# Performance work log

Measured on AMD Instinct MI355X. Metric: run time of the kernel, lower is better.

The kernel has to match this reference:

```python
import jax, jax.numpy as jnp
import numpy as np

NUM_ITEMS = 100000
HIDDEN = 128
NNZ = 1600000


def setup_inputs() -> dict:
    key = jax.random.key(0)
    k1, k2, k3, k4, k5, k6 = jax.random.split(key, 6)
    item_embedding_table = jax.random.normal(k1, (NUM_ITEMS, HIDDEN), dtype=jnp.float32)
    adj_rows = jnp.sort(jax.random.randint(k2, (NNZ,), 0, NUM_ITEMS, dtype=jnp.int32))
    adj_cols = jax.random.randint(k3, (NNZ,), 0, NUM_ITEMS, dtype=jnp.int32)
    adj_vals = jax.random.uniform(k4, (NNZ,), dtype=jnp.float32)
    # nn.Linear default init (uniform in +-1/sqrt(fan_in)) approximated by scaled normal
    W_weight = jax.random.normal(k5, (HIDDEN, HIDDEN), dtype=jnp.float32) / np.sqrt(HIDDEN)
    W_bias = jax.random.normal(k6, (HIDDEN,), dtype=jnp.float32) * 0.01
    return {
        "item_embedding_table": item_embedding_table,
        "adj_rows": adj_rows,
        "adj_cols": adj_cols,
        "adj_vals": adj_vals,
        "W_weight": W_weight,
        "W_bias": W_bias,
    }


def reference(item_embedding_table, adj_rows, adj_cols, adj_vals, W_weight, W_bias):
    # support = W(x): x @ W^T + b   (nn.Linear convention: weight [out, in])
    support = jnp.einsum("nd,hd->nh", item_embedding_table, W_weight) + W_bias  # [N, H]
    # output = sparse_coo(adj) @ support, via gather + segment-sum scatter
    msgs = adj_vals[:, None] * support[adj_cols]  # [nnz, H]
    output = jax.ops.segment_sum(msgs, adj_rows, num_segments=NUM_ITEMS)  # [N, H]
    return output
```

## Files before the change

kernel.cpp:

```cpp
#include <hip/hip_runtime.h>
#include <hip/hip_fp16.h>

#define N_ITEMS 100000
#define HID 128
#define NNZ_T 1600000
#define PREPW_BLOCKS 64
#define RP_BLOCKS 391

typedef unsigned short ushort_t;
typedef unsigned int uint_t;
typedef short bf16x8 __attribute__((ext_vector_type(8)));
typedef float f32x4 __attribute__((ext_vector_type(4)));

static __device__ __forceinline__ ushort_t f32_to_bf16(float f) {
    uint_t u = __float_as_uint(f);
    uint_t r = (u + 0x7FFFu + ((u >> 16) & 1u)) >> 16;
    return (ushort_t)r;
}

__global__ void prep(const float* __restrict__ W, const int* __restrict__ rows,
                     ushort_t* __restrict__ Wb, int* __restrict__ row_ptr) {
    if (blockIdx.x < PREPW_BLOCKS) {
        int i = blockIdx.x * 256 + threadIdx.x;
        Wb[i] = f32_to_bf16(W[i]);
        return;
    }
    int r = (blockIdx.x - PREPW_BLOCKS) * 256 + threadIdx.x;
    if (r > N_ITEMS) return;
    int lo = 0, hi = NNZ_T;
    while (lo < hi) {
        int mid = (lo + hi) >> 1;
        if (rows[mid] < r) lo = mid + 1; else hi = mid;
    }
    row_ptr[r] = lo;
}

__global__ __launch_bounds__(256) void gemm_mfma(
    const float* __restrict__ X, const ushort_t* __restrict__ Wb,
    const float* __restrict__ bias, ushort_t* __restrict__ S) {
    const int lane = threadIdx.x & 63;
    const int wave = threadIdx.x >> 6;
    const int m = lane & 15;
    const int q = lane >> 4;
    const int row0 = blockIdx.x * 64 + wave * 16;

    int arow = row0 + m;
    if (arow >= N_ITEMS) arow = N_ITEMS - 1;

    f32x4 acc[8] = {};

#pragma unroll
    for (int kb = 0; kb < 4; ++kb) {
        const int k0 = kb * 32 + q * 8;
        float4 a0 = *(const float4*)&X[(size_t)arow * HID + k0];
        float4 a1 = *(const float4*)&X[(size_t)arow * HID + k0 + 4];
        bf16x8 xf;
        xf[0] = (short)f32_to_bf16(a0.x); xf[1] = (short)f32_to_bf16(a0.y);
        xf[2] = (short)f32_to_bf16(a0.z); xf[3] = (short)f32_to_bf16(a0.w);
        xf[4] = (short)f32_to_bf16(a1.x); xf[5] = (short)f32_to_bf16(a1.y);
        xf[6] = (short)f32_to_bf16(a1.z); xf[7] = (short)f32_to_bf16(a1.w);
#pragma unroll
        for (int nt = 0; nt < 8; ++nt) {
            bf16x8 wf = *(const bf16x8*)&Wb[(size_t)(nt * 16 + m) * HID + k0];
            acc[nt] = __builtin_amdgcn_mfma_f32_16x16x32_bf16(wf, xf, acc[nt], 0, 0, 0);
        }
    }

    const int srow = row0 + m;
    const bool ok = srow < N_ITEMS;
#pragma unroll
    for (int nt = 0; nt < 8; ++nt) {
        const int c0 = nt * 16 + q * 4;
        float4 bv = *(const float4*)&bias[c0];
        ushort_t h0 = __half_as_ushort(__float2half(acc[nt][0] + bv.x));
        ushort_t h1 = __half_as_ushort(__float2half(acc[nt][1] + bv.y));
        ushort_t h2 = __half_as_ushort(__float2half(acc[nt][2] + bv.z));
        ushort_t h3 = __half_as_ushort(__float2half(acc[nt][3] + bv.w));
        uint2 pk;
        pk.x = (uint_t)h0 | ((uint_t)h1 << 16);
        pk.y = (uint_t)h2 | ((uint_t)h3 << 16);
        if (ok) *(uint2*)&S[(size_t)srow * HID + c0] = pk;
    }
}

__global__ __launch_bounds__(256) void spmm_csr(
    const int* __restrict__ cols, const float* __restrict__ vals,
    const int* __restrict__ row_ptr, const ushort_t* __restrict__ S,
    float* __restrict__ out) {
    const int lane = threadIdx.x & 63;
    const int row = blockIdx.x * 4 + ((threadIdx.x >> 6) & 3);
    if (row >= N_ITEMS) return;

    const int g = lane >> 4;
    const int l = lane & 15;

    const int p0 = row_ptr[row];
    const int p1 = row_ptr[row + 1];

    __half2 acch[4];
    acch[0] = __float2half2_rn(0.f); acch[1] = __float2half2_rn(0.f);
    acch[2] = __float2half2_rn(0.f); acch[3] = __float2half2_rn(0.f);

    for (int w0 = p0; w0 < p1; w0 += 64) {
        const int nw = min(64, p1 - w0);
        const int idx = w0 + lane;
        const int c_l = cols[min(idx, p1 - 1)];
        const float v_l = (idx < p1) ? vals[idx] : 0.f;

        for (int s0 = 0; s0 < nw; s0 += 16) {
            uint4 u[4]; float v[4];
#pragma unroll
            for (int t = 0; t < 4; ++t) {
                const int slot = s0 + 4 * t + g;
                const int c = __shfl(c_l, slot, 64);
                v[t] = __shfl(v_l, slot, 64);
                u[t] = *(const uint4*)&S[(size_t)c * HID + 8 * l];
            }
#pragma unroll
            for (int t = 0; t < 4; ++t) {
                const __half2 vv = __float2half2_rn(v[t]);
                acch[0] = __hfma2(vv, *(const __half2*)&u[t].x, acch[0]);
                acch[1] = __hfma2(vv, *(const __half2*)&u[t].y, acch[1]);
                acch[2] = __hfma2(vv, *(const __half2*)&u[t].z, acch[2]);
                acch[3] = __hfma2(vv, *(const __half2*)&u[t].w, acch[3]);
            }
        }
    }

    float acc[8];
#pragma unroll
    for (int j = 0; j < 4; ++j) {
        acc[2 * j]     = __low2float(acch[j]);
        acc[2 * j + 1] = __high2float(acch[j]);
    }
#pragma unroll
    for (int e = 0; e < 8; ++e) {
        acc[e] += __shfl_xor(acc[e], 16, 64);
        acc[e] += __shfl_xor(acc[e], 32, 64);
    }
    if (g == 0) {
        float* p = &out[(size_t)row * HID + 8 * l];
        *(float4*)p       = make_float4(acc[0], acc[1], acc[2], acc[3]);
        *(float4*)(p + 4) = make_float4(acc[4], acc[5], acc[6], acc[7]);
    }
}

extern "C" void kernel_launch(void* const* d_in, const int* in_sizes, int n_in,
                              void* d_out, int out_size, void* d_ws, size_t ws_size,
                              hipStream_t stream) {
    const float* X    = (const float*)d_in[0];
    const int*   rows = (const int*)  d_in[1];
    const int*   cols = (const int*)  d_in[2];
    const float* vals = (const float*)d_in[3];
    const float* W    = (const float*)d_in[4];
    const float* bias = (const float*)d_in[5];
    float* out = (float*)d_out;

    ushort_t* Wb      = (ushort_t*)d_ws;
    ushort_t* S       = Wb + HID * HID;
    int*      row_ptr = (int*)(S + (size_t)N_ITEMS * HID);

    prep<<<PREPW_BLOCKS + RP_BLOCKS, 256, 0, stream>>>(W, rows, Wb, row_ptr);
    gemm_mfma<<<(N_ITEMS + 63) / 64, 256, 0, stream>>>(X, Wb, bias, S);
    spmm_csr<<<(N_ITEMS + 3) / 4, 256, 0, stream>>>(cols, vals, row_ptr, S, out);
}
```

Measured before the change: 204.7 us.

## Process two CSR rows per wavefront in SpMM with interleaved gathers

The SpMM kernel now gives each wavefront two adjacent output rows instead of one. Each half of the wave loads 16 column indices and values for its row. The wave then issues eight gather loads per iteration, four for each row, into separate half-precision accumulators. This is meant to raise memory-level parallelism per wave and halve the number of waves launched. The cost is extra registers, and padded gathers on the shorter row while the longer one finishes.

```diff
diff --git a/kernel.cpp b/kernel.cpp
--- a/kernel.cpp
+++ b/kernel.cpp
@@ -88,60 +88,81 @@
     const int* __restrict__ row_ptr, const ushort_t* __restrict__ S,
     float* __restrict__ out) {
     const int lane = threadIdx.x & 63;
-    const int row = blockIdx.x * 4 + ((threadIdx.x >> 6) & 3);
-    if (row >= N_ITEMS) return;
+    const int wid = blockIdx.x * 4 + ((threadIdx.x >> 6) & 3);
+    const int r0 = wid * 2;
+    if (r0 >= N_ITEMS) return;
 
     const int g = lane >> 4;
     const int l = lane & 15;
+    const int sel = lane >> 5;
 
-    const int p0 = row_ptr[row];
-    const int p1 = row_ptr[row + 1];
+    const int2 p01 = *(const int2*)&row_ptr[r0];
+    const int pEb = row_ptr[r0 + 2];
+    int pa = p01.x; const int pEa = p01.y;
+    int pb = p01.y;
 
-    __half2 acch[4];
-    acch[0] = __float2half2_rn(0.f); acch[1] = __float2half2_rn(0.f);
-    acch[2] = __float2half2_rn(0.f); acch[3] = __float2half2_rn(0.f);
+    __half2 accA[4], accB[4];
+#pragma unroll
+    for (int j = 0; j < 4; ++j) { accA[j] = __float2half2_rn(0.f); accB[j] = __float2half2_rn(0.f); }
 
-    for (int w0 = p0; w0 < p1; w0 += 64) {
-        const int nw = min(64, p1 - w0);
-        const int idx = w0 + lane;
-        const int c_l = cols[min(idx, p1 - 1)];
-        const float v_l = (idx < p1) ? vals[idx] : 0.f;
+    while (pa < pEa || pb < pEb) {
+        const int base = sel ? pb : pa;
+        const int end  = sel ? pEb : pEa;
+        const int idx  = base + (lane & 15);
+        const int cidx = max(min(idx, end - 1), 0);
+        const int c_l  = cols[cidx];
+        const float v_l = (idx < end) ? vals[cidx] : 0.f;
 
-        for (int s0 = 0; s0 < nw; s0 += 16) {
-            uint4 u[4]; float v[4];
+        uint4 uA[4], uB[4];
+        float vA[4], vB[4];
 #pragma unroll
-            for (int t = 0; t < 4; ++t) {
-                const int slot = s0 + 4 * t + g;
-                const int c = __shfl(c_l, slot, 64);
-                v[t] = __shfl(v_l, slot, 64);
-                u[t] = *(const uint4*)&S[(size_t)c * HID + 8 * l];
-            }
+        for (int t = 0; t < 4; ++t) {
+            const int sa = 4 * t + g;
+            const int ca = __shfl(c_l, sa, 64);
+            vA[t] = __shfl(v_l, sa, 64);
+            uA[t] = *(const uint4*)&S[(size_t)ca * HID + 8 * l];
+            const int cb = __shfl(c_l, 32 + sa, 64);
+            vB[t] = __shfl(v_l, 32 + sa, 64);
+            uB[t] = *(const uint4*)&S[(size_t)cb * HID + 8 * l];
+        }
 #pragma unroll
-            for (int t = 0; t < 4; ++t) {
-                const __half2 vv = __float2half2_rn(v[t]);
-                acch[0] = __hfma2(vv, *(const __half2*)&u[t].x, acch[0]);
-                acch[1] = __hfma2(vv, *(const __half2*)&u[t].y, acch[1]);
-                acch[2] = __hfma2(vv, *(const __half2*)&u[t].z, acch[2]);
-                acch[3] = __hfma2(vv, *(const __half2*)&u[t].w, acch[3]);
-            }
+        for (int t = 0; t < 4; ++t) {
+            const __half2 wa = __float2half2_rn(vA[t]);
+            accA[0] = __hfma2(wa, *(const __half2*)&uA[t].x, accA[0]);
+            accA[1] = __hfma2(wa, *(const __half2*)&uA[t].y, accA[1]);
+            accA[2] = __hfma2(wa, *(const __half2*)&uA[t].z, accA[2]);
+            accA[3] = __hfma2(wa, *(const __half2*)&uA[t].w, accA[3]);
+            const __half2 wb = __float2half2_rn(vB[t]);
+            accB[0] = __hfma2(wb, *(const __half2*)&uB[t].x, accB[0]);
+            accB[1] = __hfma2(wb, *(const __half2*)&uB[t].y, accB[1]);
+            accB[2] = __hfma2(wb, *(const __half2*)&uB[t].z, accB[2]);
+            accB[3] = __hfma2(wb, *(const __half2*)&uB[t].w, accB[3]);
         }
+        pa = min(pa + 16, pEa);
+        pb = min(pb + 16, pEb);
     }
 
-    float acc[8];
+    float fA[8], fB[8];
 #pragma unroll
     for (int j = 0; j < 4; ++j) {
-        acc[2 * j]     = __low2float(acch[j]);
-        acc[2 * j + 1] = __high2float(acch[j]);
+        fA[2 * j] = __low2float(accA[j]);  fA[2 * j + 1] = __high2float(accA[j]);
+        fB[2 * j] = __low2float(accB[j]);  fB[2 * j + 1] = __high2float(accB[j]);
     }
 #pragma unroll
     for (int e = 0; e < 8; ++e) {
-        acc[e] += __shfl_xor(acc[e], 16, 64);
-        acc[e] += __shfl_xor(acc[e], 32, 64);
+        fA[e] += __shfl_xor(fA[e], 16, 64);
+        fA[e] += __shfl_xor(fA[e], 32, 64);
+        fB[e] += __shfl_xor(fB[e], 16, 64);
+        fB[e] += __shfl_xor(fB[e], 32, 64);
     }
     if (g == 0) {
-        float* p = &out[(size_t)row * HID + 8 * l];
-        *(float4*)p       = make_float4(acc[0], acc[1], acc[2], acc[3]);
-        *(float4*)(p + 4) = make_float4(acc[4], acc[5], acc[6], acc[7]);
+        float* p = &out[(size_t)r0 * HID + 8 * l];
+        *(float4*)p       = make_float4(fA[0], fA[1], fA[2], fA[3]);
+        *(float4*)(p + 4) = make_float4(fA[4], fA[5], fA[6], fA[7]);
+    } else if (g == 1 && r0 + 1 < N_ITEMS) {
+        float* p = &out[(size_t)(r0 + 1) * HID + 8 * l];
+        *(float4*)p       = make_float4(fB[0], fB[1], fB[2], fB[3]);
+        *(float4*)(p + 4) = make_float4(fB[4], fB[5], fB[6], fB[7]);
     }
 }
 
@@ -162,5 +183,5 @@
 
     prep<<<PREPW_BLOCKS + RP_BLOCKS, 256, 0, stream>>>(W, rows, Wb, row_ptr);
     gemm_mfma<<<(N_ITEMS + 63) / 64, 256, 0, stream>>>(X, Wb, bias, S);
-    spmm_csr<<<(N_ITEMS + 3) / 4, 256, 0, stream>>>(cols, vals, row_ptr, S, out);
+    spmm_csr<<<(N_ITEMS / 2 + 3) / 4, 256, 0, stream>>>(cols, vals, row_ptr, S, out);
 }
```

Result: no change. 203.1 us (-0.8%).
